# Kernel optimization log

Hardware: AMD Instinct MI355X
Metric: run time of the kernel (lower is better)

Reference implementation:

```python
import jax, jax.numpy as jnp
import numpy as np

THRESHOLD = 0.2
NEG_POS_RATIO = 3
ALPHA = 1.0
B, M, P, C = 64, 50, 24564, 2


def cxcy_to_xy(c):
    return jnp.concatenate([c[..., :2] - c[..., 2:] / 2, c[..., :2] + c[..., 2:] / 2], axis=-1)


def xy_to_cxcy(x):
    return jnp.concatenate([(x[..., :2] + x[..., 2:]) / 2, x[..., 2:] - x[..., :2]], axis=-1)


def cxcy_to_gcxgcy(c, p):
    # SSD encoding: offsets scaled by 10, sizes (log) scaled by 5
    return jnp.concatenate([(c[..., :2] - p[..., :2]) / (p[..., 2:] / 10.0),
                            jnp.log(c[..., 2:] / p[..., 2:]) * 5.0], axis=-1)


def jaccard(a, b):
    # a: (M,4) xy boxes, b: (P,4) xy boxes -> (M,P) IoU
    lt = jnp.maximum(a[:, None, :2], b[None, :, :2])
    rb = jnp.minimum(a[:, None, 2:], b[None, :, 2:])
    inter = jnp.prod(jnp.clip(rb - lt, 0.0), axis=-1)
    area_a = jnp.prod(a[:, 2:] - a[:, :2], axis=-1)
    area_b = jnp.prod(b[:, 2:] - b[:, :2], axis=-1)
    return inter / (area_a[:, None] + area_b[None, :] - inter)


def setup_inputs() -> dict:
    key = jax.random.key(0)
    k1, k2, k3, k4, k5, k6 = jax.random.split(key, 6)
    predicted_locs = jax.random.normal(k1, (B, P, 4), dtype=jnp.float32)
    predicted_scores = jax.random.normal(k2, (B, P, C), dtype=jnp.float32)
    # valid GT corner boxes in [0,1]: x2>x1, y2>y1
    xy1 = jax.random.uniform(k3, (B, M, 2), minval=0.0, maxval=0.75)
    wh = jax.random.uniform(k4, (B, M, 2), minval=0.05, maxval=0.25)
    boxes = jnp.concatenate([xy1, xy1 + wh], axis=-1).astype(jnp.float32)
    # priors in cxcywh with positive sizes
    pc = jax.random.uniform(k5, (P, 2), minval=0.0, maxval=1.0)
    pwh = jax.random.uniform(k6, (P, 2), minval=0.02, maxval=0.3)
    priors_cxcy = jnp.concatenate([pc, pwh], axis=-1).astype(jnp.float32)
    return {"predicted_locs": predicted_locs, "predicted_scores": predicted_scores,
            "boxes": boxes, "priors_cxcy": priors_cxcy}


def reference(predicted_locs, predicted_scores, boxes, priors_cxcy):
    n_priors = priors_cxcy.shape[0]
    priors_xy = cxcy_to_xy(priors_cxcy)

    def assign(boxes_i):  # boxes_i: (M,4) xy
        overlap = jaccard(boxes_i, priors_xy)  # (M,P)
        overlap_for_each_prior = overlap.max(axis=0)        # (P,)
        object_for_each_prior = overlap.argmax(axis=0)      # (P,)
        prior_for_each_object = overlap.argmax(axis=1)      # (M,)
        # force each object's best prior to be assigned to that object
        object_for_each_prior = object_for_each_prior.at[prior_for_each_object].set(jnp.arange(boxes_i.shape[0]))
        overlap_for_each_prior = overlap_for_each_prior.at[prior_for_each_object].set(1.0)
        labels = jnp.where(overlap_for_each_prior < THRESHOLD, 0, 1).astype(jnp.int32)
        true_locs = cxcy_to_gcxgcy(xy_to_cxcy(boxes_i[object_for_each_prior]), priors_cxcy)
        return labels, true_locs

    true_classes, true_locs = jax.vmap(assign)(boxes)  # (B,P), (B,P,4)
    pos = true_classes != 0                            # (B,P)
    n_pos = pos.sum(axis=1)                            # (B,)
    total_pos = n_pos.sum().astype(jnp.float32)

    # L1Loss(mean) over the positive-prior coordinates
    loc_abs = jnp.abs(predicted_locs - true_locs)
    loc_loss = jnp.sum(loc_abs * pos[..., None]) / (total_pos * 4.0)

    # per-prior cross entropy
    logp = jax.nn.log_softmax(predicted_scores, axis=-1)
    conf_all = -jnp.take_along_axis(logp, true_classes[..., None].astype(jnp.int32), axis=-1)[..., 0]  # (B,P)
    conf_pos_sum = jnp.sum(conf_all * pos)

    # hard negative mining: zero positives, sort descending, take top 3*n_pos per image
    conf_neg = jnp.where(pos, 0.0, conf_all)
    conf_neg_sorted = -jnp.sort(-conf_neg, axis=1)
    ranks = jnp.arange(n_priors)[None, :]
    hard = ranks < (NEG_POS_RATIO * n_pos)[:, None]
    conf_hard_sum = jnp.sum(conf_neg_sorted * hard)

    conf_loss = (conf_hard_sum + conf_pos_sum) / total_pos
    return conf_loss + ALPHA * loc_loss
```

## Files before the change

kernel.cpp:

```cpp
#include <hip/hip_runtime.h>
#include <math.h>

#define BB 64
#define MM 50
#define PP 24564
#define NBLK 96
#define THRESH 0.2f
#define P4 (PP / 4)
#define SLACK 64u
#define NCH 24
#define WMARG 0.151f
#define RCPM 8u

__device__ __forceinline__ float l1loc(float4 bxm, float4 pc, float4 pl) {
    float cx = (bxm.x + bxm.z) * 0.5f, cy = (bxm.y + bxm.w) * 0.5f;
    float w = bxm.z - bxm.x, h = bxm.w - bxm.y;
    float g0 = (cx - pc.x) / (pc.z * 0.1f);
    float g1 = (cy - pc.y) / (pc.w * 0.1f);
    float g2 = logf(w / pc.z) * 5.0f;
    float g3 = logf(h / pc.w) * 5.0f;
    return fabsf(pl.x - g0) + fabsf(pl.y - g1) + fabsf(pl.z - g2) + fabsf(pl.w - g3);
}

__global__ void k_init(int* __restrict__ ghist, unsigned long long* __restrict__ Lm) {
    int i = blockIdx.x * 256 + threadIdx.x;
    if (i < BB * 2048) ghist[i] = 0;
    if (i < BB * MM) Lm[i] = 0x00000000FFFFFFFFull;
}

__global__ void k_main(const float4* __restrict__ boxes,
                       const float4* __restrict__ pr_cxcy,
                       const float4* __restrict__ plocs,
                       const float2* __restrict__ scores,
                       unsigned long long* __restrict__ Lm,
                       float* __restrict__ bestv,
                       int* __restrict__ bmv,
                       float* __restrict__ confneg,
                       int* __restrict__ ghist,
                       int* __restrict__ npos_part,
                       float* __restrict__ cpos_part,
                       float* __restrict__ loc_part) {
    int b = blockIdx.y;
    int p = blockIdx.x * 256 + threadIdx.x;
    int tid = threadIdx.x;
    __shared__ float4 sbox[MM];
    __shared__ float sarea[MM];
    __shared__ unsigned long long smax[MM];
    __shared__ int shist[2048];
    __shared__ int si[256];
    __shared__ float s1[256], s2[256];
    for (int i = tid; i < 2048; i += 256) shist[i] = 0;
    if (tid < MM) {
        float4 bxt = boxes[b * MM + tid];
        sbox[tid] = bxt;
        sarea[tid] = (bxt.z - bxt.x) * (bxt.w - bxt.y);
        smax[tid] = 0ull;
    }
    __syncthreads();

    int np = 0;
    float cpos = 0.0f, lloc = 0.0f;
    if (p < PP) {
        float4 pc = pr_cxcy[p];
        float px1 = pc.x - pc.z * 0.5f, py1 = pc.y - pc.w * 0.5f;
        float px2 = pc.x + pc.z * 0.5f, py2 = pc.y + pc.w * 0.5f;
        float pa = (px2 - px1) * (py2 - py1);
        float binter = 0.0f, bdenom = 1.0f;
        int bm = 0;
        for (int m = 0; m < MM; ++m) {
            float4 bxm = sbox[m];
            float lx = fmaxf(bxm.x, px1), ly = fmaxf(bxm.y, py1);
            float rx = fminf(bxm.z, px2), ry = fminf(bxm.w, py2);
            float iw = fmaxf(rx - lx, 0.0f), ih = fmaxf(ry - ly, 0.0f);
            float inter = iw * ih;
            float den = sarea[m] + pa - inter;
            float l = inter * bdenom, r = binter * den;
            if (l > r) { binter = inter; bdenom = den; bm = m; }
        }
        float q = binter / bdenom;
        size_t idx = (size_t)b * PP + p;
        bestv[idx] = q;
        bmv[idx] = bm;
        unsigned long long key =
            ((unsigned long long)__float_as_uint(q) << 32) | (unsigned int)(~p);
        atomicMax(&smax[bm], key);
        bool pos = (q >= THRESH);
        float2 sc = scores[idx];
        float mx = fmaxf(sc.x, sc.y);
        float lse = mx + logf(expf(sc.x - mx) + expf(sc.y - mx));
        float conf = pos ? (lse - sc.y) : (lse - sc.x);
        float ck = pos ? 0.0f : conf;
        confneg[idx] = ck;
        atomicAdd(&shist[__float_as_uint(ck) >> 20], 1);
        if (pos) {
            np = 1;
            cpos = conf;
            lloc = l1loc(sbox[bm], pc, plocs[idx]);
        }
    }
    si[tid] = np; s1[tid] = cpos; s2[tid] = lloc;
    __syncthreads();
    for (int s = 128; s > 0; s >>= 1) {
        if (tid < s) {
            si[tid] += si[tid + s];
            s1[tid] += s1[tid + s];
            s2[tid] += s2[tid + s];
        }
        __syncthreads();
    }
    if (tid == 0) {
        int o = b * NBLK + blockIdx.x;
        npos_part[o] = si[0];
        cpos_part[o] = s1[0];
        loc_part[o] = s2[0];
    }
    if (tid < MM) {
        unsigned long long v = smax[tid];
        if (v) atomicMax(&Lm[b * MM + tid], v);
    }
    for (int i = tid; i < 2048; i += 256) {
        int c = shist[i];
        if (c) atomicAdd(&ghist[b * 2048 + i], c);
    }
}

__global__ void k_bpo3(const float4* __restrict__ boxes,
                       const float4* __restrict__ pr_cxcy,
                       const float* __restrict__ bestv,
                       unsigned long long* __restrict__ Lm) {
    int b = blockIdx.y, c = blockIdx.x, tid = threadIdx.x;
    __shared__ float4 sbox[MM];
    __shared__ float sarea[MM];
    __shared__ unsigned thr[MM];
    __shared__ unsigned long long smax[MM];
    __shared__ unsigned sminthr;
    if (tid < MM) {
        float4 bxt = boxes[b * MM + tid];
        sbox[tid] = bxt;
        sarea[tid] = (bxt.z - bxt.x) * (bxt.w - bxt.y);
        unsigned long long L = Lm[b * MM + tid];
        smax[tid] = L;
        unsigned hi = (unsigned)(L >> 32);
        thr[tid] = (hi > SLACK) ? hi - SLACK : 0u;
    }
    __syncthreads();
    if (tid == 0) {
        unsigned mt = 0xFFFFFFFFu;
        for (int j = 0; j < MM; ++j) mt = min(mt, thr[j]);
        sminthr = mt;
    }
    __syncthreads();
    unsigned minthr = sminthr;
    volatile unsigned long long* vsm = smax;
    const float4* bv4 = (const float4*)(bestv + (size_t)b * PP);
    int i = c * 256 + tid;
    if (i < P4) {
        float4 qv = bv4[i];
        float vv[4] = {qv.x, qv.y, qv.z, qv.w};
        #pragma unroll
        for (int e = 0; e < 4; ++e) {
            unsigned qb = __float_as_uint(vv[e]);
            if (qb < minthr) continue;
            int p = 4 * i + e;
            float4 pc = pr_cxcy[p];
            float px1 = pc.x - pc.z * 0.5f, py1 = pc.y - pc.w * 0.5f;
            float px2 = pc.x + pc.z * 0.5f, py2 = pc.y + pc.w * 0.5f;
            float pa = (px2 - px1) * (py2 - py1);
            for (int j = 0; j < MM; ++j) {
                if (qb < thr[j]) continue;
                float4 bxm = sbox[j];
                if (pc.x < bxm.x - WMARG || pc.x > bxm.z + WMARG ||
                    pc.y < bxm.y - WMARG || pc.y > bxm.w + WMARG) continue;
                float lx = fmaxf(bxm.x, px1), ly = fmaxf(bxm.y, py1);
                float rx = fminf(bxm.z, px2), ry = fminf(bxm.w, py2);
                float iw = fmaxf(rx - lx, 0.0f), ih = fmaxf(ry - ly, 0.0f);
                float inter = iw * ih;
                float den = sarea[j] + pa - inter;
                float qa = inter * __builtin_amdgcn_rcpf(den);
                unsigned hi = (unsigned)(vsm[j] >> 32);
                if (__float_as_uint(qa) + RCPM < hi) continue;
                float q = inter / den;
                unsigned long long key =
                    ((unsigned long long)__float_as_uint(q) << 32) | (unsigned int)(~p);
                if (key > vsm[j]) atomicMax(&smax[j], key);
            }
        }
    }
    __syncthreads();
    if (tid < MM) atomicMax(&Lm[b * MM + tid], smax[tid]);
}

__global__ void k_fix(const float4* __restrict__ boxes,
                      const float4* __restrict__ pr_cxcy,
                      const float4* __restrict__ plocs,
                      const float2* __restrict__ scores,
                      const unsigned long long* __restrict__ Lm,
                      const float* __restrict__ bestv,
                      const int* __restrict__ bmv,
                      float* __restrict__ confneg,
                      int* __restrict__ ghist,
                      int* __restrict__ npfix,
                      float* __restrict__ cposfix,
                      float* __restrict__ llocfix) {
    int b = blockIdx.x;
    int lane = threadIdx.x;
    int fp = -1;
    if (lane < MM) fp = (int)(~(unsigned)(Lm[b * MM + lane] & 0xFFFFFFFFull));
    bool active = (lane < MM);
    for (int m2 = 0; m2 < MM; ++m2) {
        int v = __shfl(fp, m2);
        if (m2 > lane && v == fp) active = false;
    }
    int dnp = 0;
    float dcp = 0.0f, dll = 0.0f;
    if (active) {
        size_t idx = (size_t)b * PP + fp;
        float bo = bestv[idx];
        bool npold = (bo >= THRESH);
        float4 pc = pr_cxcy[fp];
        float4 pl = plocs[idx];
        float llnew = l1loc(boxes[b * MM + lane], pc, pl);
        if (npold) {
            dll = llnew - l1loc(boxes[b * MM + bmv[idx]], pc, pl);
        } else {
            float2 sc = scores[idx];
            float mx = fmaxf(sc.x, sc.y);
            float lse = mx + logf(expf(sc.x - mx) + expf(sc.y - mx));
            dnp = 1;
            dcp = lse - sc.y;
            dll = llnew;
            float cold = confneg[idx];
            atomicAdd(&ghist[b * 2048 + (int)(__float_as_uint(cold) >> 20)], -1);
            atomicAdd(&ghist[b * 2048 + 0], 1);
            confneg[idx] = 0.0f;
        }
    }
    #pragma unroll
    for (int off = 32; off > 0; off >>= 1) {
        dnp += __shfl_xor(dnp, off);
        dcp += __shfl_xor(dcp, off);
        dll += __shfl_xor(dll, off);
    }
    if (lane == 0) { npfix[b] = dnp; cposfix[b] = dcp; llocfix[b] = dll; }
}

__device__ __forceinline__ float block_sum(float v, float* fred, int tid) {
    fred[tid] = v;
    __syncthreads();
    for (int s = 128; s > 0; s >>= 1) {
        if (tid < s) fred[tid] += fred[tid + s];
        __syncthreads();
    }
    float r = fred[0];
    __syncthreads();
    return r;
}

template <int NB>
__device__ __forceinline__ void suffix_find(const int* __restrict__ h, int K, int tid,
                                            int* iscr, int* bcast, int slot) {
    const int c = NB / 256;
    const int base = tid * c;
    int tsum = 0;
    #pragma unroll
    for (int i = 0; i < c; ++i) tsum += h[base + i];
    iscr[tid] = tsum;
    __syncthreads();
    int val = tsum;
    for (int off = 1; off < 256; off <<= 1) {
        int other = (tid + off < 256) ? iscr[tid + off] : 0;
        __syncthreads();
        val += other;
        iscr[tid] = val;
        __syncthreads();
    }
    int acc = val - tsum;
    int best = -1, cg = 0;
    for (int i = base + c - 1; i >= base; --i) {
        int s = acc + h[i];
        if (s >= K) { best = i; cg = acc; break; }
        acc = s;
    }
    iscr[tid] = best;
    __syncthreads();
    for (int s2 = 128; s2 > 0; s2 >>= 1) {
        if (tid < s2) iscr[tid] = max(iscr[tid], iscr[tid + s2]);
        __syncthreads();
    }
    int gbest = iscr[0];
    __syncthreads();
    if (best == gbest && best >= 0) { bcast[slot] = gbest; bcast[slot + 1] = cg; }
    __syncthreads();
}

__global__ void k_select(const float* __restrict__ confneg,
                         const int* __restrict__ ghist,
                         const int* __restrict__ npos_part,
                         const int* __restrict__ npfix,
                         float* __restrict__ chard) {
    int b = blockIdx.x, tid = threadIdx.x;
    __shared__ int h[2048];
    __shared__ float store[4096];
    __shared__ float fred[256];
    __shared__ int iscr[256];
    __shared__ int bcast[8];

    iscr[tid] = (tid < NBLK) ? npos_part[b * NBLK + tid] : 0;
    __syncthreads();
    for (int s = 128; s > 0; s >>= 1) {
        if (tid < s) iscr[tid] += iscr[tid + s];
        __syncthreads();
    }
    int npos = iscr[0] + npfix[b];
    __syncthreads();
    long long Kl = 3LL * npos;
    int K = (Kl > PP) ? PP : (int)Kl;
    if (K == 0) {
        if (tid == 0) chard[b] = 0.0f;
        return;
    }

    for (int i = tid; i < 2048; i += 256) h[i] = ghist[b * 2048 + i];
    __syncthreads();
    suffix_find<2048>(h, K, tid, iscr, bcast, 0);
    int b1 = bcast[0];
    int K1 = K - bcast[1];
    int h1cnt = h[b1];
    bool docollect = (h1cnt <= 4096);
    __syncthreads();

    for (int i = tid; i < 1024; i += 256) h[i] = 0;
    if (tid == 0) bcast[6] = 0;
    __syncthreads();
    const float4* cn4 = (const float4*)(confneg + (size_t)b * PP);
    float sa = 0.0f;
    for (int i = tid; i < P4; i += 256) {
        float4 q = cn4[i];
        float vv[4] = {q.x, q.y, q.z, q.w};
        #pragma unroll
        for (int j = 0; j < 4; ++j) {
            unsigned k = __float_as_uint(vv[j]);
            int t11 = (int)(k >> 20);
            if (t11 > b1) sa += vv[j];
            else if (t11 == b1) {
                atomicAdd(&h[(k >> 10) & 1023], 1);
                if (docollect) {
                    int ix = atomicAdd(&bcast[6], 1);
                    store[ix] = vv[j];
                }
            }
        }
    }
    float Sa = block_sum(sa, fred, tid);
    suffix_find<1024>(h, K1, tid, iscr, bcast, 2);
    int b2 = bcast[2];
    int K2 = K1 - bcast[3];
    unsigned top21 = ((unsigned)b1 << 10) | (unsigned)b2;
    __syncthreads();

    float Sb, Sc;
    int b3, K3;
    if (docollect) {
        for (int i = tid; i < 1024; i += 256) h[i] = 0;
        __syncthreads();
        float sb = 0.0f;
        for (int i = tid; i < h1cnt; i += 256) {
            unsigned k = __float_as_uint(store[i]);
            int n10 = (int)((k >> 10) & 1023);
            if (n10 > b2) sb += store[i];
            else if (n10 == b2) atomicAdd(&h[k & 1023], 1);
        }
        Sb = block_sum(sb, fred, tid);
        suffix_find<1024>(h, K2, tid, iscr, bcast, 4);
        b3 = bcast[4];
        K3 = K2 - bcast[5];
        float sc = 0.0f;
        for (int i = tid; i < h1cnt; i += 256) {
            unsigned k = __float_as_uint(store[i]);
            if ((k >> 10) == top21 && (k & 1023) > (unsigned)b3) sc += store[i];
        }
        Sc = block_sum(sc, fred, tid);
    } else {
        for (int i = tid; i < 1024; i += 256) h[i] = 0;
        __syncthreads();
        float sb = 0.0f;
        for (int i = tid; i < P4; i += 256) {
            float4 q = cn4[i];
            float vv[4] = {q.x, q.y, q.z, q.w};
            #pragma unroll
            for (int j = 0; j < 4; ++j) {
                unsigned k = __float_as_uint(vv[j]);
                if ((int)(k >> 20) == b1) {
                    int n10 = (int)((k >> 10) & 1023);
                    if (n10 > b2) sb += vv[j];
                    else if (n10 == b2) atomicAdd(&h[k & 1023], 1);
                }
            }
        }
        Sb = block_sum(sb, fred, tid);
        suffix_find<1024>(h, K2, tid, iscr, bcast, 4);
        b3 = bcast[4];
        K3 = K2 - bcast[5];
        float sc = 0.0f;
        for (int i = tid; i < P4; i += 256) {
            float4 q = cn4[i];
            float vv[4] = {q.x, q.y, q.z, q.w};
            #pragma unroll
            for (int j = 0; j < 4; ++j) {
                unsigned k = __float_as_uint(vv[j]);
                if ((k >> 10) == top21 && (k & 1023) > (unsigned)b3) sc += vv[j];
            }
        }
        Sc = block_sum(sc, fred, tid);
    }
    if (tid == 0) {
        unsigned kstar = (top21 << 10) | (unsigned)b3;
        chard[b] = Sa + Sb + Sc + (float)K3 * __uint_as_float(kstar);
    }
}

__global__ void k_final(const int* __restrict__ npos_part,
                        const float* __restrict__ cpos_part,
                        const float* __restrict__ loc_part,
                        const float* __restrict__ chard,
                        const int* __restrict__ npfix,
                        const float* __restrict__ cposfix,
                        const float* __restrict__ llocfix,
                        float* __restrict__ out) {
    __shared__ int si[256];
    __shared__ float s1[256], s2[256], s3[256];
    int tn = 0; float tc = 0.0f, tl = 0.0f, th = 0.0f;
    for (int i = threadIdx.x; i < BB * NBLK; i += 256) {
        tn += npos_part[i];
        tc += cpos_part[i];
        tl += loc_part[i];
    }
    if (threadIdx.x < BB) {
        th = chard[threadIdx.x];
        tn += npfix[threadIdx.x];
        tc += cposfix[threadIdx.x];
        tl += llocfix[threadIdx.x];
    }
    si[threadIdx.x] = tn; s1[threadIdx.x] = tc; s2[threadIdx.x] = tl; s3[threadIdx.x] = th;
    __syncthreads();
    for (int s = 128; s > 0; s >>= 1) {
        if (threadIdx.x < s) {
            si[threadIdx.x] += si[threadIdx.x + s];
            s1[threadIdx.x] += s1[threadIdx.x + s];
            s2[threadIdx.x] += s2[threadIdx.x + s];
            s3[threadIdx.x] += s3[threadIdx.x + s];
        }
        __syncthreads();
    }
    if (threadIdx.x == 0) {
        float tp = (float)si[0];
        out[0] = (s3[0] + s1[0]) / tp + s2[0] / (tp * 4.0f);
    }
}

extern "C" void kernel_launch(void* const* d_in, const int* in_sizes, int n_in,
                              void* d_out, int out_size, void* d_ws, size_t ws_size,
                              hipStream_t stream) {
    const float4* plocs   = (const float4*)d_in[0];
    const float2* scores  = (const float2*)d_in[1];
    const float4* boxes   = (const float4*)d_in[2];
    const float4* priors  = (const float4*)d_in[3];
    float* out = (float*)d_out;

    char* ws = (char*)d_ws;
    size_t off = 0;
    auto alloc = [&](size_t bytes) -> void* {
        void* p = ws + off;
        off += (bytes + 255) & ~(size_t)255;
        return p;
    };
    float*              confneg = (float*) alloc((size_t)BB * PP * 4);
    float*              bestv   = (float*) alloc((size_t)BB * PP * 4);
    int*                bmv     = (int*)   alloc((size_t)BB * PP * 4);
    int*                ghist   = (int*)   alloc((size_t)BB * 2048 * 4);
    unsigned long long* Lm      = (unsigned long long*)alloc((size_t)BB * MM * 8);
    int*                npos_p  = (int*)   alloc((size_t)BB * NBLK * 4);
    float*              cpos_p  = (float*) alloc((size_t)BB * NBLK * 4);
    float*              loc_p   = (float*) alloc((size_t)BB * NBLK * 4);
    float*              chard   = (float*) alloc((size_t)BB * 4);
    int*                npfix   = (int*)   alloc((size_t)BB * 4);
    float*              cposfix = (float*) alloc((size_t)BB * 4);
    float*              llocfix = (float*) alloc((size_t)BB * 4);
    (void)ws_size; (void)in_sizes; (void)n_in; (void)out_size;

    k_init<<<512, 256, 0, stream>>>(ghist, Lm);
    k_main<<<dim3(NBLK, BB), 256, 0, stream>>>(boxes, priors, plocs, scores,
                                               Lm, bestv, bmv, confneg, ghist,
                                               npos_p, cpos_p, loc_p);
    k_bpo3<<<dim3(NCH, BB), 256, 0, stream>>>(boxes, priors, bestv, Lm);
    k_fix<<<BB, 64, 0, stream>>>(boxes, priors, plocs, scores, Lm, bestv, bmv,
                                 confneg, ghist, npfix, cposfix, llocfix);
    k_select<<<BB, 256, 0, stream>>>(confneg, ghist, npos_p, npfix, chard);
    k_final<<<1, 256, 0, stream>>>(npos_p, cpos_p, loc_p, chard,
                                   npfix, cposfix, llocfix, out);
}
```

Measured before the change: 140.3 us.

## Split selection across chunked blocks, fuse fix into select, two priors per thread

The selection stage previously ran one block per image and scanned all of confneg serially. It is now split into k_selKF (fix plus first histogram level), k_selA (8 chunks per image that accumulate the second-level histogram and compact candidates into a global store), and k_selB (finishes the radix select). k_fix is folded into the select kernel, which applies its histogram adjustments in shared memory. k_main now processes two priors per thread, and k_bpo3 sorts boxes by threshold so its inner loop can break early. This trades one extra launch and global atomics and scratch for more parallelism in the selection pass.

```diff
diff --git a/kernel.cpp b/kernel.cpp
--- a/kernel.cpp
+++ b/kernel.cpp
@@ -4,13 +4,17 @@
 #define BB 64
 #define MM 50
 #define PP 24564
-#define NBLK 96
+#define PPT 2
+#define NBLK2 48
 #define THRESH 0.2f
 #define P4 (PP / 4)
 #define SLACK 64u
 #define NCH 24
 #define WMARG 0.151f
 #define RCPM 8u
+#define SELCH 8
+#define SCH4 ((P4 + SELCH - 1) / SELCH)
+#define CAP PP
 
 __device__ __forceinline__ float l1loc(float4 bxm, float4 pc, float4 pl) {
     float cx = (bxm.x + bxm.z) * 0.5f, cy = (bxm.y + bxm.w) * 0.5f;
@@ -22,9 +26,12 @@
     return fabsf(pl.x - g0) + fabsf(pl.y - g1) + fabsf(pl.z - g2) + fabsf(pl.w - g3);
 }
 
-__global__ void k_init(int* __restrict__ ghist, unsigned long long* __restrict__ Lm) {
+__global__ void k_init(int* __restrict__ ghist, int* __restrict__ ghist2,
+                       int* __restrict__ gcur, unsigned long long* __restrict__ Lm) {
     int i = blockIdx.x * 256 + threadIdx.x;
     if (i < BB * 2048) ghist[i] = 0;
+    if (i < BB * 1024) ghist2[i] = 0;
+    if (i < BB) gcur[i] = 0;
     if (i < BB * MM) Lm[i] = 0x00000000FFFFFFFFull;
 }
 
@@ -41,8 +48,11 @@
                        float* __restrict__ cpos_part,
                        float* __restrict__ loc_part) {
     int b = blockIdx.y;
-    int p = blockIdx.x * 256 + threadIdx.x;
     int tid = threadIdx.x;
+    int p0 = blockIdx.x * 512 + tid;
+    int p1 = p0 + 256;
+    bool v0 = (p0 < PP), v1 = (p1 < PP);
+    int q0i = v0 ? p0 : PP - 1, q1i = v1 ? p1 : PP - 1;
     __shared__ float4 sbox[MM];
     __shared__ float sarea[MM];
     __shared__ unsigned long long smax[MM];
@@ -58,32 +68,47 @@
     }
     __syncthreads();
 
+    float4 pcA = pr_cxcy[q0i], pcB = pr_cxcy[q1i];
+    float ax1 = pcA.x - pcA.z * 0.5f, ay1 = pcA.y - pcA.w * 0.5f;
+    float ax2 = pcA.x + pcA.z * 0.5f, ay2 = pcA.y + pcA.w * 0.5f;
+    float aa = (ax2 - ax1) * (ay2 - ay1);
+    float bx1 = pcB.x - pcB.z * 0.5f, by1 = pcB.y - pcB.w * 0.5f;
+    float bx2 = pcB.x + pcB.z * 0.5f, by2 = pcB.y + pcB.w * 0.5f;
+    float ab = (bx2 - bx1) * (by2 - by1);
+    float biA = 0.0f, bdA = 1.0f, biB = 0.0f, bdB = 1.0f;
+    int bmA = 0, bmB = 0;
+    for (int m = 0; m < MM; ++m) {
+        float4 bxm = sbox[m];
+        float am = sarea[m];
+        {
+            float lx = fmaxf(bxm.x, ax1), ly = fmaxf(bxm.y, ay1);
+            float rx = fminf(bxm.z, ax2), ry = fminf(bxm.w, ay2);
+            float iw = fmaxf(rx - lx, 0.0f), ih = fmaxf(ry - ly, 0.0f);
+            float inter = iw * ih;
+            float den = am + aa - inter;
+            float l = inter * bdA, r = biA * den;
+            if (l > r) { biA = inter; bdA = den; bmA = m; }
+        }
+        {
+            float lx = fmaxf(bxm.x, bx1), ly = fmaxf(bxm.y, by1);
+            float rx = fminf(bxm.z, bx2), ry = fminf(bxm.w, by2);
+            float iw = fmaxf(rx - lx, 0.0f), ih = fmaxf(ry - ly, 0.0f);
+            float inter = iw * ih;
+            float den = am + ab - inter;
+            float l = inter * bdB, r = biB * den;
+            if (l > r) { biB = inter; bdB = den; bmB = m; }
+        }
+    }
     int np = 0;
     float cpos = 0.0f, lloc = 0.0f;
-    if (p < PP) {
-        float4 pc = pr_cxcy[p];
-        float px1 = pc.x - pc.z * 0.5f, py1 = pc.y - pc.w * 0.5f;
-        float px2 = pc.x + pc.z * 0.5f, py2 = pc.y + pc.w * 0.5f;
-        float pa = (px2 - px1) * (py2 - py1);
-        float binter = 0.0f, bdenom = 1.0f;
-        int bm = 0;
-        for (int m = 0; m < MM; ++m) {
-            float4 bxm = sbox[m];
-            float lx = fmaxf(bxm.x, px1), ly = fmaxf(bxm.y, py1);
-            float rx = fminf(bxm.z, px2), ry = fminf(bxm.w, py2);
-            float iw = fmaxf(rx - lx, 0.0f), ih = fmaxf(ry - ly, 0.0f);
-            float inter = iw * ih;
-            float den = sarea[m] + pa - inter;
-            float l = inter * bdenom, r = binter * den;
-            if (l > r) { binter = inter; bdenom = den; bm = m; }
-        }
-        float q = binter / bdenom;
-        size_t idx = (size_t)b * PP + p;
+    if (v0) {
+        float q = biA / bdA;
+        size_t idx = (size_t)b * PP + p0;
         bestv[idx] = q;
-        bmv[idx] = bm;
+        bmv[idx] = bmA;
         unsigned long long key =
-            ((unsigned long long)__float_as_uint(q) << 32) | (unsigned int)(~p);
-        atomicMax(&smax[bm], key);
+            ((unsigned long long)__float_as_uint(q) << 32) | (unsigned int)(~p0);
+        atomicMax(&smax[bmA], key);
         bool pos = (q >= THRESH);
         float2 sc = scores[idx];
         float mx = fmaxf(sc.x, sc.y);
@@ -92,11 +117,25 @@
         float ck = pos ? 0.0f : conf;
         confneg[idx] = ck;
         atomicAdd(&shist[__float_as_uint(ck) >> 20], 1);
-        if (pos) {
-            np = 1;
-            cpos = conf;
-            lloc = l1loc(sbox[bm], pc, plocs[idx]);
-        }
+        if (pos) { np++; cpos += conf; lloc += l1loc(sbox[bmA], pcA, plocs[idx]); }
+    }
+    if (v1) {
+        float q = biB / bdB;
+        size_t idx = (size_t)b * PP + p1;
+        bestv[idx] = q;
+        bmv[idx] = bmB;
+        unsigned long long key =
+            ((unsigned long long)__float_as_uint(q) << 32) | (unsigned int)(~p1);
+        atomicMax(&smax[bmB], key);
+        bool pos = (q >= THRESH);
+        float2 sc = scores[idx];
+        float mx = fmaxf(sc.x, sc.y);
+        float lse = mx + logf(expf(sc.x - mx) + expf(sc.y - mx));
+        float conf = pos ? (lse - sc.y) : (lse - sc.x);
+        float ck = pos ? 0.0f : conf;
+        confneg[idx] = ck;
+        atomicAdd(&shist[__float_as_uint(ck) >> 20], 1);
+        if (pos) { np++; cpos += conf; lloc += l1loc(sbox[bmB], pcB, plocs[idx]); }
     }
     si[tid] = np; s1[tid] = cpos; s2[tid] = lloc;
     __syncthreads();
@@ -109,7 +148,7 @@
         __syncthreads();
     }
     if (tid == 0) {
-        int o = b * NBLK + blockIdx.x;
+        int o = b * NBLK2 + blockIdx.x;
         npos_part[o] = si[0];
         cpos_part[o] = s1[0];
         loc_part[o] = s2[0];
@@ -132,6 +171,7 @@
     __shared__ float4 sbox[MM];
     __shared__ float sarea[MM];
     __shared__ unsigned thr[MM];
+    __shared__ unsigned char order[MM];
     __shared__ unsigned long long smax[MM];
     __shared__ unsigned sminthr;
     if (tid < MM) {
@@ -144,6 +184,15 @@
         thr[tid] = (hi > SLACK) ? hi - SLACK : 0u;
     }
     __syncthreads();
+    if (tid < MM) {
+        unsigned tj = thr[tid];
+        int rank = 0;
+        for (int k = 0; k < MM; ++k) {
+            unsigned tk = thr[k];
+            if (tk < tj || (tk == tj && k < tid)) rank++;
+        }
+        order[rank] = (unsigned char)tid;
+    }
     if (tid == 0) {
         unsigned mt = 0xFFFFFFFFu;
         for (int j = 0; j < MM; ++j) mt = min(mt, thr[j]);
@@ -166,8 +215,9 @@
             float px1 = pc.x - pc.z * 0.5f, py1 = pc.y - pc.w * 0.5f;
             float px2 = pc.x + pc.z * 0.5f, py2 = pc.y + pc.w * 0.5f;
             float pa = (px2 - px1) * (py2 - py1);
-            for (int j = 0; j < MM; ++j) {
-                if (qb < thr[j]) continue;
+            for (int jj = 0; jj < MM; ++jj) {
+                int j = (int)order[jj];
+                if (thr[j] > qb) break;
                 float4 bxm = sbox[j];
                 if (pc.x < bxm.x - WMARG || pc.x > bxm.z + WMARG ||
                     pc.y < bxm.y - WMARG || pc.y > bxm.w + WMARG) continue;
@@ -190,60 +240,6 @@
     if (tid < MM) atomicMax(&Lm[b * MM + tid], smax[tid]);
 }
 
-__global__ void k_fix(const float4* __restrict__ boxes,
-                      const float4* __restrict__ pr_cxcy,
-                      const float4* __restrict__ plocs,
-                      const float2* __restrict__ scores,
-                      const unsigned long long* __restrict__ Lm,
-                      const float* __restrict__ bestv,
-                      const int* __restrict__ bmv,
-                      float* __restrict__ confneg,
-                      int* __restrict__ ghist,
-                      int* __restrict__ npfix,
-                      float* __restrict__ cposfix,
-                      float* __restrict__ llocfix) {
-    int b = blockIdx.x;
-    int lane = threadIdx.x;
-    int fp = -1;
-    if (lane < MM) fp = (int)(~(unsigned)(Lm[b * MM + lane] & 0xFFFFFFFFull));
-    bool active = (lane < MM);
-    for (int m2 = 0; m2 < MM; ++m2) {
-        int v = __shfl(fp, m2);
-        if (m2 > lane && v == fp) active = false;
-    }
-    int dnp = 0;
-    float dcp = 0.0f, dll = 0.0f;
-    if (active) {
-        size_t idx = (size_t)b * PP + fp;
-        float bo = bestv[idx];
-        bool npold = (bo >= THRESH);
-        float4 pc = pr_cxcy[fp];
-        float4 pl = plocs[idx];
-        float llnew = l1loc(boxes[b * MM + lane], pc, pl);
-        if (npold) {
-            dll = llnew - l1loc(boxes[b * MM + bmv[idx]], pc, pl);
-        } else {
-            float2 sc = scores[idx];
-            float mx = fmaxf(sc.x, sc.y);
-            float lse = mx + logf(expf(sc.x - mx) + expf(sc.y - mx));
-            dnp = 1;
-            dcp = lse - sc.y;
-            dll = llnew;
-            float cold = confneg[idx];
-            atomicAdd(&ghist[b * 2048 + (int)(__float_as_uint(cold) >> 20)], -1);
-            atomicAdd(&ghist[b * 2048 + 0], 1);
-            confneg[idx] = 0.0f;
-        }
-    }
-    #pragma unroll
-    for (int off = 32; off > 0; off >>= 1) {
-        dnp += __shfl_xor(dnp, off);
-        dcp += __shfl_xor(dcp, off);
-        dll += __shfl_xor(dll, off);
-    }
-    if (lane == 0) { npfix[b] = dnp; cposfix[b] = dcp; llocfix[b] = dll; }
-}
-
 __device__ __forceinline__ float block_sum(float v, float* fred, int tid) {
     fred[tid] = v;
     __syncthreads();
@@ -293,126 +289,195 @@
     __syncthreads();
 }
 
-__global__ void k_select(const float* __restrict__ confneg,
-                         const int* __restrict__ ghist,
-                         const int* __restrict__ npos_part,
-                         const int* __restrict__ npfix,
-                         float* __restrict__ chard) {
+__global__ void k_selKF(const float4* __restrict__ boxes,
+                        const float4* __restrict__ pr_cxcy,
+                        const float4* __restrict__ plocs,
+                        const float2* __restrict__ scores,
+                        const unsigned long long* __restrict__ Lm,
+                        const float* __restrict__ bestv,
+                        const int* __restrict__ bmv,
+                        float* __restrict__ confneg,
+                        const int* __restrict__ ghist,
+                        const int* __restrict__ npos_part,
+                        int4* __restrict__ selp,
+                        int* __restrict__ npfix,
+                        float* __restrict__ cposfix,
+                        float* __restrict__ llocfix) {
     int b = blockIdx.x, tid = threadIdx.x;
     __shared__ int h[2048];
-    __shared__ float store[4096];
-    __shared__ float fred[256];
     __shared__ int iscr[256];
     __shared__ int bcast[8];
-
-    iscr[tid] = (tid < NBLK) ? npos_part[b * NBLK + tid] : 0;
+    __shared__ int s_dnp;
+    for (int i = tid; i < 2048; i += 256) h[i] = ghist[b * 2048 + i];
+    __syncthreads();
+    if (tid < 64) {
+        int fp = -1;
+        if (tid < MM) fp = (int)(~(unsigned)(Lm[b * MM + tid] & 0xFFFFFFFFull));
+        bool active = (tid < MM);
+        for (int m2 = 0; m2 < MM; ++m2) {
+            int v = __shfl(fp, m2);
+            if (m2 > tid && v == fp) active = false;
+        }
+        int dnp = 0;
+        float dcp = 0.0f, dll = 0.0f;
+        if (active) {
+            size_t idx = (size_t)b * PP + fp;
+            float bo = bestv[idx];
+            bool npold = (bo >= THRESH);
+            float4 pc = pr_cxcy[fp];
+            float4 pl = plocs[idx];
+            float llnew = l1loc(boxes[b * MM + tid], pc, pl);
+            if (npold) {
+                dll = llnew - l1loc(boxes[b * MM + bmv[idx]], pc, pl);
+            } else {
+                float2 sc = scores[idx];
+                float mx = fmaxf(sc.x, sc.y);
+                float lse = mx + logf(expf(sc.x - mx) + expf(sc.y - mx));
+                dnp = 1;
+                dcp = lse - sc.y;
+                dll = llnew;
+                float cold = confneg[idx];
+                atomicAdd(&h[(int)(__float_as_uint(cold) >> 20)], -1);
+                atomicAdd(&h[0], 1);
+                confneg[idx] = 0.0f;
+            }
+        }
+        #pragma unroll
+        for (int off = 32; off > 0; off >>= 1) {
+            dnp += __shfl_xor(dnp, off);
+            dcp += __shfl_xor(dcp, off);
+            dll += __shfl_xor(dll, off);
+        }
+        if (tid == 0) {
+            s_dnp = dnp;
+            npfix[b] = dnp; cposfix[b] = dcp; llocfix[b] = dll;
+        }
+    }
+    __syncthreads();
+    iscr[tid] = (tid < NBLK2) ? npos_part[b * NBLK2 + tid] : 0;
     __syncthreads();
     for (int s = 128; s > 0; s >>= 1) {
         if (tid < s) iscr[tid] += iscr[tid + s];
         __syncthreads();
     }
-    int npos = iscr[0] + npfix[b];
+    int npos = iscr[0] + s_dnp;
     __syncthreads();
     long long Kl = 3LL * npos;
     int K = (Kl > PP) ? PP : (int)Kl;
     if (K == 0) {
-        if (tid == 0) chard[b] = 0.0f;
+        if (tid == 0) selp[b] = make_int4(0, -1, 0, 0);
         return;
     }
-
-    for (int i = tid; i < 2048; i += 256) h[i] = ghist[b * 2048 + i];
-    __syncthreads();
     suffix_find<2048>(h, K, tid, iscr, bcast, 0);
-    int b1 = bcast[0];
-    int K1 = K - bcast[1];
-    int h1cnt = h[b1];
-    bool docollect = (h1cnt <= 4096);
-    __syncthreads();
-
-    for (int i = tid; i < 1024; i += 256) h[i] = 0;
-    if (tid == 0) bcast[6] = 0;
-    __syncthreads();
-    const float4* cn4 = (const float4*)(confneg + (size_t)b * PP);
+    if (tid == 0) {
+        int b1 = bcast[0];
+        selp[b] = make_int4(K, b1, K - bcast[1], h[b1]);
+    }
+}
+
+__global__ void k_selA(const float* __restrict__ confneg,
+                       const int4* __restrict__ selp,
+                       float* __restrict__ saP,
+                       int* __restrict__ ghist2,
+                       int* __restrict__ gcur,
+                       float* __restrict__ gstore) {
+    int b = blockIdx.y, c = blockIdx.x, tid = threadIdx.x;
+    __shared__ float fred[256];
+    __shared__ int h2[1024];
+    __shared__ float sstore[SCH4 * 4];
+    __shared__ int scnt, sbase;
+    for (int i = tid; i < 1024; i += 256) h2[i] = 0;
+    if (tid == 0) scnt = 0;
+    __syncthreads();
+    int4 sp = selp[b];
+    int b1 = sp.y;
     float sa = 0.0f;
-    for (int i = tid; i < P4; i += 256) {
-        float4 q = cn4[i];
-        float vv[4] = {q.x, q.y, q.z, q.w};
-        #pragma unroll
-        for (int j = 0; j < 4; ++j) {
-            unsigned k = __float_as_uint(vv[j]);
-            int t11 = (int)(k >> 20);
-            if (t11 > b1) sa += vv[j];
-            else if (t11 == b1) {
-                atomicAdd(&h[(k >> 10) & 1023], 1);
-                if (docollect) {
-                    int ix = atomicAdd(&bcast[6], 1);
-                    store[ix] = vv[j];
-                }
-            }
-        }
-    }
-    float Sa = block_sum(sa, fred, tid);
-    suffix_find<1024>(h, K1, tid, iscr, bcast, 2);
-    int b2 = bcast[2];
-    int K2 = K1 - bcast[3];
-    unsigned top21 = ((unsigned)b1 << 10) | (unsigned)b2;
-    __syncthreads();
-
-    float Sb, Sc;
-    int b3, K3;
-    if (docollect) {
-        for (int i = tid; i < 1024; i += 256) h[i] = 0;
-        __syncthreads();
-        float sb = 0.0f;
-        for (int i = tid; i < h1cnt; i += 256) {
-            unsigned k = __float_as_uint(store[i]);
-            int n10 = (int)((k >> 10) & 1023);
-            if (n10 > b2) sb += store[i];
-            else if (n10 == b2) atomicAdd(&h[k & 1023], 1);
-        }
-        Sb = block_sum(sb, fred, tid);
-        suffix_find<1024>(h, K2, tid, iscr, bcast, 4);
-        b3 = bcast[4];
-        K3 = K2 - bcast[5];
-        float sc = 0.0f;
-        for (int i = tid; i < h1cnt; i += 256) {
-            unsigned k = __float_as_uint(store[i]);
-            if ((k >> 10) == top21 && (k & 1023) > (unsigned)b3) sc += store[i];
-        }
-        Sc = block_sum(sc, fred, tid);
-    } else {
-        for (int i = tid; i < 1024; i += 256) h[i] = 0;
-        __syncthreads();
-        float sb = 0.0f;
-        for (int i = tid; i < P4; i += 256) {
+    if (b1 >= 0) {
+        const float4* cn4 = (const float4*)(confneg + (size_t)b * PP);
+        int i1 = min((c + 1) * SCH4, P4);
+        for (int i = c * SCH4 + tid; i < i1; i += 256) {
             float4 q = cn4[i];
             float vv[4] = {q.x, q.y, q.z, q.w};
             #pragma unroll
             for (int j = 0; j < 4; ++j) {
                 unsigned k = __float_as_uint(vv[j]);
-                if ((int)(k >> 20) == b1) {
-                    int n10 = (int)((k >> 10) & 1023);
-                    if (n10 > b2) sb += vv[j];
-                    else if (n10 == b2) atomicAdd(&h[k & 1023], 1);
+                int t11 = (int)(k >> 20);
+                if (t11 > b1) sa += vv[j];
+                else if (t11 == b1) {
+                    atomicAdd(&h2[(k >> 10) & 1023], 1);
+                    int ix = atomicAdd(&scnt, 1);
+                    sstore[ix] = vv[j];
                 }
             }
         }
-        Sb = block_sum(sb, fred, tid);
-        suffix_find<1024>(h, K2, tid, iscr, bcast, 4);
-        b3 = bcast[4];
-        K3 = K2 - bcast[5];
-        float sc = 0.0f;
-        for (int i = tid; i < P4; i += 256) {
-            float4 q = cn4[i];
-            float vv[4] = {q.x, q.y, q.z, q.w};
-            #pragma unroll
-            for (int j = 0; j < 4; ++j) {
-                unsigned k = __float_as_uint(vv[j]);
-                if ((k >> 10) == top21 && (k & 1023) > (unsigned)b3) sc += vv[j];
-            }
-        }
-        Sc = block_sum(sc, fred, tid);
-    }
+    }
+    __syncthreads();
+    if (tid == 0 && scnt > 0) sbase = atomicAdd(&gcur[b], scnt);
+    __syncthreads();
+    int n = scnt;
+    for (int i = tid; i < n; i += 256)
+        gstore[(size_t)b * CAP + sbase + i] = sstore[i];
+    for (int i = tid; i < 1024; i += 256) {
+        int v = h2[i];
+        if (v) atomicAdd(&ghist2[b * 1024 + i], v);
+    }
+    float Sa = block_sum(sa, fred, tid);
+    if (tid == 0) saP[b * SELCH + c] = Sa;
+}
+
+__global__ void k_selB(const int4* __restrict__ selp,
+                       const float* __restrict__ saP,
+                       const int* __restrict__ ghist2,
+                       const float* __restrict__ gstore,
+                       float* __restrict__ chard) {
+    int b = blockIdx.x, tid = threadIdx.x;
+    __shared__ int h[1024];
+    __shared__ float fred[256];
+    __shared__ int iscr[256];
+    __shared__ int bcast[8];
+    __shared__ float sSa;
+    int4 sp = selp[b];
+    if (sp.x == 0) {
+        if (tid == 0) chard[b] = 0.0f;
+        return;
+    }
+    int b1 = sp.y, K1 = sp.z, h1cnt = sp.w;
+    if (tid == 0) {
+        float s = 0.0f;
+        for (int j = 0; j < SELCH; ++j) s += saP[b * SELCH + j];
+        sSa = s;
+    }
+    for (int i = tid; i < 1024; i += 256) h[i] = ghist2[b * 1024 + i];
+    __syncthreads();
+    float Sa = sSa;
+    suffix_find<1024>(h, K1, tid, iscr, bcast, 0);
+    int b2 = bcast[0];
+    int K2 = K1 - bcast[1];
+    unsigned top21 = ((unsigned)b1 << 10) | (unsigned)b2;
+    __syncthreads();
+
+    const float* gs = gstore + (size_t)b * CAP;
+    for (int i = tid; i < 1024; i += 256) h[i] = 0;
+    __syncthreads();
+    float sb = 0.0f;
+    for (int i = tid; i < h1cnt; i += 256) {
+        float v = gs[i];
+        unsigned k = __float_as_uint(v);
+        int n10 = (int)((k >> 10) & 1023);
+        if (n10 > b2) sb += v;
+        else if (n10 == b2) atomicAdd(&h[k & 1023], 1);
+    }
+    float Sb = block_sum(sb, fred, tid);
+    suffix_find<1024>(h, K2, tid, iscr, bcast, 2);
+    int b3 = bcast[2];
+    int K3 = K2 - bcast[3];
+    float sc = 0.0f;
+    for (int i = tid; i < h1cnt; i += 256) {
+        float v = gs[i];
+        unsigned k = __float_as_uint(v);
+        if ((k >> 10) == top21 && (k & 1023) > (unsigned)b3) sc += v;
+    }
+    float Sc = block_sum(sc, fred, tid);
     if (tid == 0) {
         unsigned kstar = (top21 << 10) | (unsigned)b3;
         chard[b] = Sa + Sb + Sc + (float)K3 * __uint_as_float(kstar);
@@ -430,7 +495,7 @@
     __shared__ int si[256];
     __shared__ float s1[256], s2[256], s3[256];
     int tn = 0; float tc = 0.0f, tl = 0.0f, th = 0.0f;
-    for (int i = threadIdx.x; i < BB * NBLK; i += 256) {
+    for (int i = threadIdx.x; i < BB * NBLK2; i += 256) {
         tn += npos_part[i];
         tc += cpos_part[i];
         tl += loc_part[i];
@@ -478,24 +543,31 @@
     float*              bestv   = (float*) alloc((size_t)BB * PP * 4);
     int*                bmv     = (int*)   alloc((size_t)BB * PP * 4);
     int*                ghist   = (int*)   alloc((size_t)BB * 2048 * 4);
+    int*                ghist2  = (int*)   alloc((size_t)BB * 1024 * 4);
     unsigned long long* Lm      = (unsigned long long*)alloc((size_t)BB * MM * 8);
-    int*                npos_p  = (int*)   alloc((size_t)BB * NBLK * 4);
-    float*              cpos_p  = (float*) alloc((size_t)BB * NBLK * 4);
-    float*              loc_p   = (float*) alloc((size_t)BB * NBLK * 4);
+    int*                npos_p  = (int*)   alloc((size_t)BB * NBLK2 * 4);
+    float*              cpos_p  = (float*) alloc((size_t)BB * NBLK2 * 4);
+    float*              loc_p   = (float*) alloc((size_t)BB * NBLK2 * 4);
     float*              chard   = (float*) alloc((size_t)BB * 4);
     int*                npfix   = (int*)   alloc((size_t)BB * 4);
     float*              cposfix = (float*) alloc((size_t)BB * 4);
     float*              llocfix = (float*) alloc((size_t)BB * 4);
+    int4*               selp    = (int4*)  alloc((size_t)BB * 16);
+    float*              saP     = (float*) alloc((size_t)BB * SELCH * 4);
+    int*                gcur    = (int*)   alloc((size_t)BB * 4);
+    float*              gstore  = (float*) alloc((size_t)BB * CAP * 4);
     (void)ws_size; (void)in_sizes; (void)n_in; (void)out_size;
 
-    k_init<<<512, 256, 0, stream>>>(ghist, Lm);
-    k_main<<<dim3(NBLK, BB), 256, 0, stream>>>(boxes, priors, plocs, scores,
-                                               Lm, bestv, bmv, confneg, ghist,
-                                               npos_p, cpos_p, loc_p);
+    k_init<<<512, 256, 0, stream>>>(ghist, ghist2, gcur, Lm);
+    k_main<<<dim3(NBLK2, BB), 256, 0, stream>>>(boxes, priors, plocs, scores,
+                                                Lm, bestv, bmv, confneg, ghist,
+                                                npos_p, cpos_p, loc_p);
     k_bpo3<<<dim3(NCH, BB), 256, 0, stream>>>(boxes, priors, bestv, Lm);
-    k_fix<<<BB, 64, 0, stream>>>(boxes, priors, plocs, scores, Lm, bestv, bmv,
-                                 confneg, ghist, npfix, cposfix, llocfix);
-    k_select<<<BB, 256, 0, stream>>>(confneg, ghist, npos_p, npfix, chard);
+    k_selKF<<<BB, 256, 0, stream>>>(boxes, priors, plocs, scores, Lm, bestv, bmv,
+                                    confneg, ghist, npos_p, selp,
+                                    npfix, cposfix, llocfix);
+    k_selA<<<dim3(SELCH, BB), 256, 0, stream>>>(confneg, selp, saP, ghist2, gcur, gstore);
+    k_selB<<<BB, 256, 0, stream>>>(selp, saP, ghist2, gstore, chard);
     k_final<<<1, 256, 0, stream>>>(npos_p, cpos_p, loc_p, chard,
                                    npfix, cposfix, llocfix, out);
 }
```

Measured after the change: 152.1 us. 1.08x slower.
